# Kernel optimization log

Hardware: AMD Instinct MI355X
Metric: run time of the kernel (lower is better)

## Reference

```python
import jax, jax.numpy as jnp
import numpy as np

DIM = 4096
X_H_SCALE = 1.0
HAD_SCALE = 1.0 / np.sqrt(DIM)  # orthonormal FWHT normalization


def fwht(x):
    """Fast Walsh-Hadamard transform along the last axis (Sylvester order).
    x: [..., N] with N a power of 2. O(N log N) butterfly, fully vectorized
    over all leading dims; the loop is over the fixed log2(N) stages only.
    """
    n = x.shape[-1]
    stages = int(np.log2(n))
    assert 1 << stages == n, "last dim must be a power of 2"
    lead = x.shape[:-1]
    for i in range(stages):
        blk = 1 << i  # block size doubling each stage
        y = x.reshape(lead + (n // (2 * blk), 2, blk))
        a = y[..., 0, :]
        b = y[..., 1, :]
        x = jnp.concatenate([a + b, a - b], axis=-1).reshape(lead + (n,))
    return x


def setup_inputs() -> dict:
    key = jax.random.key(0)
    x = jax.random.normal(key, (4, 2048, DIM), dtype=jnp.float32)
    return {"x": x}


def reference(x):
    # forward: qx = FWHT(x) * (had_scale / x_H_scale)
    scale = jnp.asarray(HAD_SCALE / X_H_SCALE, dtype=x.dtype)
    return fwht(x) * scale
```

## Files before the change

### kernel.cpp

```cpp
#include <hip/hip_runtime.h>

#define DIM 4096
#define HAD_SCALE 0.015625f

__device__ __forceinline__ int swz(int a) {
    return a ^ (((a >> 6) & 7) << 2);
}

__device__ __forceinline__ void fwht16(float r[16]) {
#pragma unroll
    for (int s = 1; s < 16; s <<= 1) {
#pragma unroll
        for (int i = 0; i < 16; i++) {
            if ((i & s) == 0) {
                float a = r[i];
                float b = r[i ^ s];
                r[i]     = a + b;
                r[i ^ s] = a - b;
            }
        }
    }
}

__global__ __launch_bounds__(256) void fwht_kernel(const float* __restrict__ x,
                                                   float* __restrict__ y) {
    __shared__ float lds[DIM];
    const int t = threadIdx.x;
    const size_t row = blockIdx.x;
    const float* xin = x + row * DIM;
    float* yout = y + row * DIM;

    float r[16];

    const float4* __restrict__ x4 = (const float4*)xin;
#pragma unroll
    for (int c = 0; c < 4; c++) {
        float4 v = x4[c * 256 + t];
        r[4 * c + 0] = v.x;
        r[4 * c + 1] = v.y;
        r[4 * c + 2] = v.z;
        r[4 * c + 3] = v.w;
    }
    fwht16(r);

#pragma unroll
    for (int c = 0; c < 4; c++) {
        int a = swz(4 * t + 1024 * c);
        *(float4*)&lds[a] = make_float4(r[4 * c + 0], r[4 * c + 1],
                                        r[4 * c + 2], r[4 * c + 3]);
    }
    __syncthreads();

    const int baseB = (t & 3) + ((t >> 2) << 6);
#pragma unroll
    for (int m = 0; m < 16; m++) r[m] = lds[swz(baseB + (m << 2))];
    fwht16(r);
#pragma unroll
    for (int m = 0; m < 16; m++) lds[swz(baseB + (m << 2))] = r[m];
    __syncthreads();

    const int baseC = (t & 63) + ((t >> 6) << 10);
#pragma unroll
    for (int m = 0; m < 16; m++) r[m] = lds[swz(baseC + (m << 6))];
    fwht16(r);

#pragma unroll
    for (int m = 0; m < 16; m++) yout[baseC + (m << 6)] = r[m] * HAD_SCALE;
}

extern "C" void kernel_launch(void* const* d_in, const int* in_sizes, int n_in,
                              void* d_out, int out_size, void* d_ws, size_t ws_size,
                              hipStream_t stream) {
    const float* x = (const float*)d_in[0];
    float* y = (float*)d_out;
    const int n = in_sizes[0];
    const int rows = n / DIM;
    fwht_kernel<<<rows, 256, 0, stream>>>(x, y);
}
```

Baseline: 228.4 us.

## Replace one LDS transpose pass with DPP, swizzle and shuffle butterflies

Butterfly stages for index bits 2-3 now run as cross-lane quad-permute DPP operations right after the first in-register pass. Bits 8-9 run after the second pass, using ds_swizzle and shfl_xor. This removes one full LDS store/load round trip and one barrier, leaving a single transpose through shared memory. In exchange, the output store pattern becomes 64-byte contiguous segments instead of 256-byte ones, and it adds cross-lane instruction overhead.

```diff
diff --git a/kernel.cpp b/kernel.cpp
--- a/kernel.cpp
+++ b/kernel.cpp
@@ -22,6 +22,13 @@
     }
 }
 
+template <int CTRL>
+__device__ __forceinline__ float qperm(float v) {
+    return __int_as_float(
+        __builtin_amdgcn_mov_dpp(__float_as_int(v), CTRL, 0xF, 0xF, false));
+}
+
+
 __global__ __launch_bounds__(256) void fwht_kernel(const float* __restrict__ x,
                                                    float* __restrict__ y) {
     __shared__ float lds[DIM];
@@ -43,6 +50,19 @@
     }
     fwht16(r);
 
+    const float s1 = (t & 1) ? -1.f : 1.f;
+#pragma unroll
+    for (int i = 0; i < 16; i++) {
+        float p = qperm<0xB1>(r[i]);
+        r[i] = __builtin_fmaf(r[i], s1, p);
+    }
+    const float s2 = (t & 2) ? -1.f : 1.f;
+#pragma unroll
+    for (int i = 0; i < 16; i++) {
+        float p = qperm<0x4E>(r[i]);
+        r[i] = __builtin_fmaf(r[i], s2, p);
+    }
+
 #pragma unroll
     for (int c = 0; c < 4; c++) {
         int a = swz(4 * t + 1024 * c);
@@ -51,21 +71,28 @@
     }
     __syncthreads();
 
-    const int baseB = (t & 3) + ((t >> 2) << 6);
+    const int base = (t & 15) + ((t >> 4) << 8);
 #pragma unroll
-    for (int m = 0; m < 16; m++) r[m] = lds[swz(baseB + (m << 2))];
-    fwht16(r);
-#pragma unroll
-    for (int m = 0; m < 16; m++) lds[swz(baseB + (m << 2))] = r[m];
-    __syncthreads();
-
-    const int baseC = (t & 63) + ((t >> 6) << 10);
-#pragma unroll
-    for (int m = 0; m < 16; m++) r[m] = lds[swz(baseC + (m << 6))];
+    for (int m = 0; m < 16; m++) r[m] = lds[swz(base + (m << 4))];
     fwht16(r);
 
+    const float s16 = (t & 16) ? -1.f : 1.f;
 #pragma unroll
-    for (int m = 0; m < 16; m++) yout[baseC + (m << 6)] = r[m] * HAD_SCALE;
+    for (int i = 0; i < 16; i++) {
+        float p = __int_as_float(
+            __builtin_amdgcn_ds_swizzle(__float_as_int(r[i]), 0x401F));
+        r[i] = __builtin_fmaf(r[i], s16, p);
+    }
+    const float s32 = (t & 32) ? -1.f : 1.f;
+#pragma unroll
+    for (int i = 0; i < 16; i++) {
+        float p = __shfl_xor(r[i], 32, 64);
+        r[i] = __builtin_fmaf(r[i], s32, p);
+    }
+
+#pragma unroll
+    for (int m = 0; m < 16; m++)
+        yout[base + (m << 4)] = r[m] * HAD_SCALE;
 }
 
 extern "C" void kernel_launch(void* const* d_in, const int* in_sizes, int n_in,
```

New measurement: 229.0 us. Within noise of the previous version (+0.3%).

## Replace LDS transpose stages with DPP/swizzle cross-lane butterflies and one LDS exchange

Applied to the files above, without the earlier changes.

Performs the middle Hadamard stages across lanes with DPP quad permutes, ds_swizzle and shfl_xor instead of writing to and reading back from LDS. The last two stages across waves use a single LDS write and a 4-way float4 read-combine. This removes one barrier and the scalar-strided LDS traffic, and makes the global stores coalesced float4. In exchange there are more cross-lane ops (ds_swizzle and shfl still go through the LDS crossbar) and 3x the LDS reads in the final combine.

```diff
diff --git a/kernel.cpp b/kernel.cpp
--- a/kernel.cpp
+++ b/kernel.cpp
@@ -2,10 +2,6 @@
 
 #define DIM 4096
 #define HAD_SCALE 0.015625f
-
-__device__ __forceinline__ int swz(int a) {
-    return a ^ (((a >> 6) & 7) << 2);
-}
 
 __device__ __forceinline__ void fwht16(float r[16]) {
 #pragma unroll
@@ -22,17 +18,29 @@
     }
 }
 
+template <int CTRL>
+__device__ __forceinline__ float qperm(float v) {
+    return __int_as_float(
+        __builtin_amdgcn_mov_dpp(__float_as_int(v), CTRL, 0xF, 0xF, false));
+}
+
+template <int OFS>
+__device__ __forceinline__ float lswz(float v) {
+    return __int_as_float(
+        __builtin_amdgcn_ds_swizzle(__float_as_int(v), OFS));
+}
+
+
 __global__ __launch_bounds__(256) void fwht_kernel(const float* __restrict__ x,
                                                    float* __restrict__ y) {
     __shared__ float lds[DIM];
     const int t = threadIdx.x;
     const size_t row = blockIdx.x;
-    const float* xin = x + row * DIM;
-    float* yout = y + row * DIM;
+    const float4* __restrict__ x4 = (const float4*)(x + row * DIM);
+    float4* __restrict__ y4 = (float4*)(y + row * DIM);
 
     float r[16];
 
-    const float4* __restrict__ x4 = (const float4*)xin;
 #pragma unroll
     for (int c = 0; c < 4; c++) {
         float4 v = x4[c * 256 + t];
@@ -43,29 +51,59 @@
     }
     fwht16(r);
 
+    const float sA = (t & 1) ? -1.f : 1.f;
+#pragma unroll
+    for (int i = 0; i < 16; i++)
+        r[i] = __builtin_fmaf(r[i], sA, qperm<0xB1>(r[i]));
+    const float sB = (t & 2) ? -1.f : 1.f;
+#pragma unroll
+    for (int i = 0; i < 16; i++)
+        r[i] = __builtin_fmaf(r[i], sB, qperm<0x4E>(r[i]));
+
+    const float sC = (t & 4) ? -1.f : 1.f;
+#pragma unroll
+    for (int i = 0; i < 16; i++)
+        r[i] = __builtin_fmaf(r[i], sC, lswz<0x101F>(r[i]));
+    const float sD = (t & 8) ? -1.f : 1.f;
+#pragma unroll
+    for (int i = 0; i < 16; i++)
+        r[i] = __builtin_fmaf(r[i], sD, lswz<0x201F>(r[i]));
+    const float sE = (t & 16) ? -1.f : 1.f;
+#pragma unroll
+    for (int i = 0; i < 16; i++)
+        r[i] = __builtin_fmaf(r[i], sE, lswz<0x401F>(r[i]));
+
+    const float sF = (t & 32) ? -1.f : 1.f;
+#pragma unroll
+    for (int i = 0; i < 16; i++)
+        r[i] = __builtin_fmaf(r[i], sF, __shfl_xor(r[i], 32, 64));
+
+#pragma unroll
+    for (int c = 0; c < 4; c++)
+        *(float4*)&lds[4 * t + 1024 * c] =
+            make_float4(r[4 * c + 0], r[4 * c + 1], r[4 * c + 2], r[4 * c + 3]);
+    __syncthreads();
+
+    const float s0 = (t & 64) ? -1.f : 1.f;
+    const float s1 = (t & 128) ? -1.f : 1.f;
+    const int a = 4 * t;
 #pragma unroll
     for (int c = 0; c < 4; c++) {
-        int a = swz(4 * t + 1024 * c);
-        *(float4*)&lds[a] = make_float4(r[4 * c + 0], r[4 * c + 1],
-                                        r[4 * c + 2], r[4 * c + 3]);
+        const int b = 1024 * c;
+        float4 p1 = *(const float4*)&lds[(a ^ 256) + b];
+        float4 p2 = *(const float4*)&lds[(a ^ 512) + b];
+        float4 p3 = *(const float4*)&lds[(a ^ 768) + b];
+        float4 res;
+        res.x = __builtin_fmaf(__builtin_fmaf(r[4 * c + 0], s0, p1.x), s1,
+                               __builtin_fmaf(p2.x, s0, p3.x)) * HAD_SCALE;
+        res.y = __builtin_fmaf(__builtin_fmaf(r[4 * c + 1], s0, p1.y), s1,
+                               __builtin_fmaf(p2.y, s0, p3.y)) * HAD_SCALE;
+        res.z = __builtin_fmaf(__builtin_fmaf(r[4 * c + 2], s0, p1.z), s1,
+                               __builtin_fmaf(p2.z, s0, p3.z)) * HAD_SCALE;
+        res.w = __builtin_fmaf(__builtin_fmaf(r[4 * c + 3], s0, p1.w), s1,
+                               __builtin_fmaf(p2.w, s0, p3.w)) * HAD_SCALE;
+        y4[c * 256 + t] = res;
     }
-    __syncthreads();
-
-    const int baseB = (t & 3) + ((t >> 2) << 6);
-#pragma unroll
-    for (int m = 0; m < 16; m++) r[m] = lds[swz(baseB + (m << 2))];
-    fwht16(r);
-#pragma unroll
-    for (int m = 0; m < 16; m++) lds[swz(baseB + (m << 2))] = r[m];
-    __syncthreads();
-
-    const int baseC = (t & 63) + ((t >> 6) << 10);
-#pragma unroll
-    for (int m = 0; m < 16; m++) r[m] = lds[swz(baseC + (m << 6))];
-    fwht16(r);
-
-#pragma unroll
-    for (int m = 0; m < 16; m++) yout[baseC + (m << 6)] = r[m] * HAD_SCALE;
 }
 
 extern "C" void kernel_launch(void* const* d_in, const int* in_sizes, int n_in,
```

Measured after the change: 226.5 us. About the same (-0.9%).

## Compute FWHT per wavefront with register butterflies and cross-lane DPP/swizzle exchanges

Applied to the files above, without the earlier changes.

Each wavefront now owns a full 4096-element row and keeps 64 values per lane in registers. The butterfly stages across lanes use DPP quad permutes, ds_swizzle and shfl_xor, which removes the shared-memory round trips and block-level barriers. Four rows are processed per 256-thread block, so the grid shrinks by four. The cost is much higher register pressure (64 floats per lane), which lowers occupancy, plus many cross-lane ops for the 384 exchange steps per lane.

```diff
diff --git a/kernel.cpp b/kernel.cpp
--- a/kernel.cpp
+++ b/kernel.cpp
@@ -3,15 +3,75 @@
 #define DIM 4096
 #define HAD_SCALE 0.015625f
 
-__device__ __forceinline__ int swz(int a) {
-    return a ^ (((a >> 6) & 7) << 2);
+template <int CTRL>
+__device__ __forceinline__ float qperm(float v) {
+    return __int_as_float(
+        __builtin_amdgcn_mov_dpp(__float_as_int(v), CTRL, 0xF, 0xF, false));
 }
 
-__device__ __forceinline__ void fwht16(float r[16]) {
+template <int OFS>
+__device__ __forceinline__ float lswz(float v) {
+    return __int_as_float(
+        __builtin_amdgcn_ds_swizzle(__float_as_int(v), OFS));
+}
+
+
+__global__ __launch_bounds__(256) void fwht_kernel(const float* __restrict__ x,
+                                                   float* __restrict__ y) {
+    const int t = threadIdx.x;
+    const int lane = t & 63;
+    const int w = t >> 6;
+    const size_t row = (size_t)blockIdx.x * 4 + w;
+    const float4* __restrict__ x4 = (const float4*)(x + row * DIM);
+    float4* __restrict__ y4 = (float4*)(y + row * DIM);
+
+    float r[64];
+
 #pragma unroll
-    for (int s = 1; s < 16; s <<= 1) {
+    for (int g = 0; g < 16; g++) {
+        float4 v = x4[g * 64 + lane];
+        r[4 * g + 0] = v.x;
+        r[4 * g + 1] = v.y;
+        r[4 * g + 2] = v.z;
+        r[4 * g + 3] = v.w;
+    }
+
+    const float sA = (lane & 1)  ? -1.f : 1.f;
+    const float sB = (lane & 2)  ? -1.f : 1.f;
+    const float sC = (lane & 4)  ? -1.f : 1.f;
+    const float sD = (lane & 8)  ? -1.f : 1.f;
+    const float sE = (lane & 16) ? -1.f : 1.f;
+    const float sF = (lane & 32) ? -1.f : 1.f;
+
 #pragma unroll
-        for (int i = 0; i < 16; i++) {
+    for (int g = 0; g < 16; g++) {
+        {
+            float a = r[4 * g + 0], b = r[4 * g + 1];
+            float c = r[4 * g + 2], d = r[4 * g + 3];
+            float ab0 = a + b, ab1 = a - b;
+            float cd0 = c + d, cd1 = c - d;
+            r[4 * g + 0] = ab0 + cd0;
+            r[4 * g + 1] = ab1 + cd1;
+            r[4 * g + 2] = ab0 - cd0;
+            r[4 * g + 3] = ab1 - cd1;
+        }
+#pragma unroll
+        for (int e = 0; e < 4; e++) {
+            float v = r[4 * g + e];
+            v = __builtin_fmaf(v, sA, qperm<0xB1>(v));
+            v = __builtin_fmaf(v, sB, qperm<0x4E>(v));
+            v = __builtin_fmaf(v, sC, lswz<0x101F>(v));
+            v = __builtin_fmaf(v, sD, lswz<0x201F>(v));
+            v = __builtin_fmaf(v, sE, lswz<0x401F>(v));
+            v = __builtin_fmaf(v, sF, __shfl_xor(v, 32, 64));
+            r[4 * g + e] = v;
+        }
+    }
+
+#pragma unroll
+    for (int s = 4; s < 64; s <<= 1) {
+#pragma unroll
+        for (int i = 0; i < 64; i++) {
             if ((i & s) == 0) {
                 float a = r[i];
                 float b = r[i ^ s];
@@ -20,52 +80,14 @@
             }
         }
     }
-}
-
-__global__ __launch_bounds__(256) void fwht_kernel(const float* __restrict__ x,
-                                                   float* __restrict__ y) {
-    __shared__ float lds[DIM];
-    const int t = threadIdx.x;
-    const size_t row = blockIdx.x;
-    const float* xin = x + row * DIM;
-    float* yout = y + row * DIM;
-
-    float r[16];
-
-    const float4* __restrict__ x4 = (const float4*)xin;
-#pragma unroll
-    for (int c = 0; c < 4; c++) {
-        float4 v = x4[c * 256 + t];
-        r[4 * c + 0] = v.x;
-        r[4 * c + 1] = v.y;
-        r[4 * c + 2] = v.z;
-        r[4 * c + 3] = v.w;
-    }
-    fwht16(r);
 
 #pragma unroll
-    for (int c = 0; c < 4; c++) {
-        int a = swz(4 * t + 1024 * c);
-        *(float4*)&lds[a] = make_float4(r[4 * c + 0], r[4 * c + 1],
-                                        r[4 * c + 2], r[4 * c + 3]);
+    for (int g = 0; g < 16; g++) {
+        y4[g * 64 + lane] = make_float4(r[4 * g + 0] * HAD_SCALE,
+                                        r[4 * g + 1] * HAD_SCALE,
+                                        r[4 * g + 2] * HAD_SCALE,
+                                        r[4 * g + 3] * HAD_SCALE);
     }
-    __syncthreads();
-
-    const int baseB = (t & 3) + ((t >> 2) << 6);
-#pragma unroll
-    for (int m = 0; m < 16; m++) r[m] = lds[swz(baseB + (m << 2))];
-    fwht16(r);
-#pragma unroll
-    for (int m = 0; m < 16; m++) lds[swz(baseB + (m << 2))] = r[m];
-    __syncthreads();
-
-    const int baseC = (t & 63) + ((t >> 6) << 10);
-#pragma unroll
-    for (int m = 0; m < 16; m++) r[m] = lds[swz(baseC + (m << 6))];
-    fwht16(r);
-
-#pragma unroll
-    for (int m = 0; m < 16; m++) yout[baseC + (m << 6)] = r[m] * HAD_SCALE;
 }
 
 extern "C" void kernel_launch(void* const* d_in, const int* in_sizes, int n_in,
@@ -75,5 +97,5 @@
     float* y = (float*)d_out;
     const int n = in_sizes[0];
     const int rows = n / DIM;
-    fwht_kernel<<<rows, 256, 0, stream>>>(x, y);
+    fwht_kernel<<<rows / 4, 256, 0, stream>>>(x, y);
 }
```

Result: no change. 232.6 us (+1.8%).
